# Kernel tuning notes

Measured on AMD Instinct MI355X. Metric: run time of the kernel, lower is better.

Reference implementation:

```python
import jax, jax.numpy as jnp
import numpy as np

B, N, G = 256, 512, 117  # batch, max_num_cells, n_genes
CH = 25                  # Emphsis conv out channels (hidden_d_1st_conv)


def setup_inputs() -> dict:
    key = jax.random.key(0)
    ks = jax.random.split(key, 11)
    images = jax.random.normal(ks[0], (B, N, 1, 7, 7), dtype=jnp.float32)
    spot_images = jax.random.normal(ks[1], (B, 1, 28, 28), dtype=jnp.float32)
    gene_expression = jax.random.normal(ks[2], (B, G), dtype=jnp.float32)
    # Emphsis: Conv2d(1, 25, k=3, s=1) + ReLU
    W_emph = jax.random.normal(ks[3], (CH, 1, 3, 3), dtype=jnp.float32) * 0.2
    b_emph = jax.random.normal(ks[4], (CH,), dtype=jnp.float32) * 0.1
    # 117 stacked GeneBlock Linear(625, 1) heads -> one (G, 625) matrix
    W_reg = jax.random.normal(ks[5], (G, 625), dtype=jnp.float32) * 0.04
    b_reg = jax.random.normal(ks[6], (G,), dtype=jnp.float32) * 0.1
    # PatchEmbedding: Conv2d(1, 3, k=5, s=5)
    W_patch = jax.random.normal(ks[7], (3, 1, 5, 5), dtype=jnp.float32) * 0.2
    b_patch = jax.random.normal(ks[8], (3,), dtype=jnp.float32) * 0.1
    # global_embedding: Linear(75, 1) + ELU
    W_glob = jax.random.normal(ks[9], (1, 75), dtype=jnp.float32) * 0.1
    b_glob = jax.random.normal(ks[10], (1,), dtype=jnp.float32) * 0.1
    return dict(images=images, spot_images=spot_images, gene_expression=gene_expression,
                W_emph=W_emph, b_emph=b_emph, W_reg=W_reg, b_reg=b_reg,
                W_patch=W_patch, b_patch=b_patch, W_glob=W_glob, b_glob=b_glob)


def reference(images, spot_images, gene_expression, W_emph, b_emph, W_reg, b_reg,
              W_patch, b_patch, W_glob, b_glob):
    Bn, Nc = images.shape[0], images.shape[1]
    # Emphsis conv over all (batch, cell) pairs at once: (B*N, 1, 7, 7) -> (B*N, 25, 5, 5)
    x = images.reshape(Bn * Nc, 1, 7, 7)
    t = jax.lax.conv_general_dilated(x, W_emph, window_strides=(1, 1), padding='VALID',
                                     dimension_numbers=('NCHW', 'OIHW', 'NCHW'))
    t = jax.nn.relu(t + b_emph[None, :, None, None])
    flat = t.reshape(Bn, Nc, CH * 5 * 5)  # (B, N, 625)
    # 117 independent Linear(625,1) heads fused into one matmul -> (B, N, G)
    out = jnp.einsum('bnd,gd->bng', flat, W_reg) + b_reg
    # PatchEmbedding: (B,1,28,28) -> (B,3,5,5) -> tokens (B,25,3) -> flatten (B,75)
    s = jax.lax.conv_general_dilated(spot_images, W_patch, window_strides=(5, 5), padding='VALID',
                                     dimension_numbers=('NCHW', 'OIHW', 'NCHW'))
    s = s + b_patch[None, :, None, None]
    s = s.reshape(Bn, 3, 25).transpose(0, 2, 1).reshape(Bn, 75)
    glob = jax.nn.elu(s @ W_glob.T + b_glob)  # (B, 1)
    # out1 broadcast of global embedding over (cells, genes)
    cell = jax.nn.relu(out + glob[:, :, None])  # (B, N, G)
    # F.linear with ones weight over cell axis == sum over cells
    spot = cell.sum(axis=1)  # (B, G)
    out1 = jnp.broadcast_to(glob[:, :, None], (Bn, Nc, out.shape[2]))  # (B, N, G)
    return spot, cell, out1
```

## Files before the change

kernel.cpp:

```cpp
#include <hip/hip_runtime.h>


typedef __attribute__((ext_vector_type(16))) float f32x16;
typedef __attribute__((ext_vector_type(8))) short short8;
typedef __attribute__((ext_vector_type(2))) unsigned int uint2v;
typedef __attribute__((ext_vector_type(4))) unsigned int uint4v;

#define WCOMB_OFF 0
#define GLOB_OFF  245760
#define SPOT_OFF  246784

#define SPOT_OUT_OFF 0
#define CELL_OUT_OFF 29952
#define OUT1_OUT_OFF 15365376

__device__ __forceinline__ unsigned short f2bf(float x) {
  unsigned int u = __builtin_bit_cast(unsigned int, x);
  u = (u + 0x7FFFu + ((u >> 16) & 1u)) >> 16;
  return (unsigned short)u;
}

__device__ __forceinline__ unsigned int cvt_pk_bf16(float lo, float hi) {
  unsigned int w;
  asm("v_cvt_pk_bf16_f32 %0, %1, %2" : "=v"(w) : "v"(lo), "v"(hi));
  return w;
}

__device__ __forceinline__ void gload16(const void* g, void* l) {
  __builtin_amdgcn_global_load_lds(
      (const __attribute__((address_space(1))) void*)g,
      (__attribute__((address_space(3))) void*)l, 16, 0, 0);
}

__global__ __launch_bounds__(128) void prep_kernel(
    const float* __restrict__ spot_images, const float* __restrict__ W_patch,
    const float* __restrict__ b_patch, const float* __restrict__ W_glob,
    const float* __restrict__ b_glob, const float* __restrict__ W_reg,
    const float* __restrict__ W_emph, const float* __restrict__ b_emph,
    unsigned short* __restrict__ wcomb, float* __restrict__ glob) {
  int bid = blockIdx.x;
  int tid = threadIdx.x;
  if (bid < 256) {
    __shared__ float red[75];
    if (tid < 75) {
      int token = tid / 3;
      int chan = tid - token * 3;
      int ty = token / 5, tx = token - ty * 5;
      const float* img = spot_images + bid * 784 + (ty * 5) * 28 + tx * 5;
      float a = 0.f;
      #pragma unroll
      for (int i = 0; i < 5; ++i)
        #pragma unroll
        for (int j = 0; j < 5; ++j)
          a = fmaf(img[i * 28 + j], W_patch[chan * 25 + i * 5 + j], a);
      a += b_patch[chan];
      red[tid] = a * W_glob[tid];
    }
    __syncthreads();
    if (tid == 0) {
      float s = b_glob[0];
      for (int k = 0; k < 75; ++k) s += red[k];
      glob[bid] = (s > 0.f) ? s : expm1f(s);
    }
  } else if (bid < 336) {
    int idx = bid - 256;
    int jt = idx >> 2, s = idx & 3;
    if (tid < 64) {
      int j = jt * 32 + (tid & 31);
      int h = tid >> 5;
      unsigned short hv[8];
      #pragma unroll
      for (int jj = 0; jj < 8; ++jj) {
        int i = s * 16 + h * 8 + jj;
        float val = 0.f;
        if (j < 625) {
          int ch = j / 25, p = j % 25;
          int oy = p / 5, ox = p - oy * 5;
          if (i < 49) {
            int iy = i / 7, ix = i - iy * 7;
            int ky = iy - oy, kx = ix - ox;
            if (ky >= 0 && ky < 3 && kx >= 0 && kx < 3)
              val = W_emph[ch * 9 + ky * 3 + kx];
          } else if (i == 49) {
            val = b_emph[ch];
          }
        }
        hv[jj] = f2bf(val);
      }
      unsigned int u[4];
      #pragma unroll
      for (int k = 0; k < 4; ++k)
        u[k] = (unsigned int)hv[2 * k] | ((unsigned int)hv[2 * k + 1] << 16);
      ((uint4*)wcomb)[jt * 768 + s * 64 + tid] = make_uint4(u[0], u[1], u[2], u[3]);
    }
  } else {
    int idx = bid - 336;
    int sg = idx >> 2, q = idx & 3;
    if (tid < 64) {
      int g = q * 32 + (tid & 31);
      int h = tid >> 5;
      unsigned short hv[8];
      #pragma unroll
      for (int jj = 0; jj < 8; ++jj) {
        int k = sg * 16 + h * 8 + jj;
        float val = (g < 117 && k < 625) ? W_reg[g * 625 + k] : 0.f;
        hv[jj] = f2bf(val);
      }
      unsigned int u[4];
      #pragma unroll
      for (int k = 0; k < 4; ++k)
        u[k] = (unsigned int)hv[2 * k] | ((unsigned int)hv[2 * k + 1] << 16);
      int jt = sg >> 1, c = (sg & 1) * 4 + q;
      ((uint4*)wcomb)[jt * 768 + 256 + c * 64 + tid] =
          make_uint4(u[0], u[1], u[2], u[3]);
    }
  }
}

__global__ __launch_bounds__(512) void main_kernel(
    const float* __restrict__ images, const float* __restrict__ b_reg,
    const unsigned short* __restrict__ wcomb, const float* __restrict__ glob,
    float* __restrict__ out, float* __restrict__ spotp) {
  __shared__ char smem[59392];
  unsigned short* imgbs = (unsigned short*)smem;
  char* wbuf = smem + 32768;
  float* C = (float*)smem;
  float* red = (float*)(smem + 57344);
  int tid = threadIdx.x;
  int bid = blockIdx.x;
  int b = bid >> 1, half = bid & 1;
  int n0 = half * 256;

  int l = tid & 63;
  int ct = __builtin_amdgcn_readfirstlane(tid >> 6);
  const char* wcombB = (const char*)wcomb;

  float gb = glob[b];
  size_t rowbase = (size_t)(b * 512 + n0);
  float4 gv = make_float4(gb, gb, gb, gb);
  float4* o1v = (float4*)(out + OUT1_OUT_OFF + rowbase * 117);

  auto stage = [&](int jt, int buf) {
    const char* s0 = wcombB + jt * 12288 + ct * 1024 + l * 16;
    char* d0 = wbuf + buf * 12288 + ct * 1024;
    gload16(s0, d0);
    if (ct < 4) gload16(s0 + 8192, d0 + 8192);
  };

  #pragma unroll
  for (int it = 0; it < 4; ++it) {
    int u = it * 512 + tid;
    int cell = u & 255, kc = u >> 8;
    const float* src = images + (size_t)(b * 512 + n0 + cell) * 49 + kc * 8;
    float v[8];
    #pragma unroll
    for (int j = 0; j < 8; ++j) v[j] = 0.f;
    if (kc < 6) {
      #pragma unroll
      for (int j = 0; j < 8; ++j) v[j] = src[j];
    } else if (kc == 6) {
      v[0] = src[0];
      v[1] = 1.0f;
    }
    unsigned int uu[4];
    #pragma unroll
    for (int k = 0; k < 4; ++k) uu[k] = cvt_pk_bf16(v[2 * k], v[2 * k + 1]);
    ((uint4*)imgbs)[kc * 256 + cell] = make_uint4(uu[0], uu[1], uu[2], uu[3]);
  }
  stage(0, 0);
  __syncthreads();

  int m = l & 31, hh = l >> 5;
  const short8* imgb8 = (const short8*)imgbs;

  short8 bi0 = imgb8[(0 + hh) * 256 + ct * 32 + m];
  short8 bi1 = imgb8[(2 + hh) * 256 + ct * 32 + m];
  short8 bi2 = imgb8[(4 + hh) * 256 + ct * 32 + m];
  short8 bi3 = imgb8[(6 + hh) * 256 + ct * 32 + m];

  f32x16 acc0, acc1, acc2, acc3;
  #pragma unroll
  for (int i = 0; i < 16; ++i) {
    acc0[i] = 0.f; acc1[i] = 0.f; acc2[i] = 0.f; acc3[i] = 0.f;
  }

  for (int jt = 0; jt < 20; ++jt) {
    if (jt < 19) stage(jt + 1, (jt + 1) & 1);

    if (jt < 15) {
      int idx = jt * 512 + tid;
      if (idx < 7488) o1v[idx] = gv;
    }

    const short8* wB = (const short8*)(wbuf + (jt & 1) * 12288);
    short8 a0 = wB[l];
    short8 a1 = wB[64 + l];
    short8 a2 = wB[128 + l];
    short8 a3 = wB[192 + l];

    f32x16 o;
    #pragma unroll
    for (int i = 0; i < 16; ++i) o[i] = 0.f;
    o = __builtin_amdgcn_mfma_f32_32x32x16_bf16(a0, bi0, o, 0, 0, 0);
    o = __builtin_amdgcn_mfma_f32_32x32x16_bf16(a1, bi1, o, 0, 0, 0);
    o = __builtin_amdgcn_mfma_f32_32x32x16_bf16(a2, bi2, o, 0, 0, 0);
    o = __builtin_amdgcn_mfma_f32_32x32x16_bf16(a3, bi3, o, 0, 0, 0);

    unsigned int W[8];
    #pragma unroll
    for (int q = 0; q < 8; ++q)
      W[q] = cvt_pk_bf16(fmaxf(o[2 * q], 0.f), fmaxf(o[2 * q + 1], 0.f));
    uint2v s02 = __builtin_amdgcn_permlane32_swap(W[0], W[2], false, false);
    uint2v s13 = __builtin_amdgcn_permlane32_swap(W[1], W[3], false, false);
    uint2v s46 = __builtin_amdgcn_permlane32_swap(W[4], W[6], false, false);
    uint2v s57 = __builtin_amdgcn_permlane32_swap(W[5], W[7], false, false);
    uint4v f0 = {s02[0], s13[0], s02[1], s13[1]};
    uint4v f1 = {s46[0], s57[0], s46[1], s57[1]};
    short8 af0 = __builtin_bit_cast(short8, f0);
    short8 af1 = __builtin_bit_cast(short8, f1);

    acc0 = __builtin_amdgcn_mfma_f32_32x32x16_bf16(af0, wB[256 + l], acc0, 0, 0, 0);
    acc1 = __builtin_amdgcn_mfma_f32_32x32x16_bf16(af0, wB[320 + l], acc1, 0, 0, 0);
    acc2 = __builtin_amdgcn_mfma_f32_32x32x16_bf16(af0, wB[384 + l], acc2, 0, 0, 0);
    acc3 = __builtin_amdgcn_mfma_f32_32x32x16_bf16(af0, wB[448 + l], acc3, 0, 0, 0);
    acc0 = __builtin_amdgcn_mfma_f32_32x32x16_bf16(af1, wB[512 + l], acc0, 0, 0, 0);
    acc1 = __builtin_amdgcn_mfma_f32_32x32x16_bf16(af1, wB[576 + l], acc1, 0, 0, 0);
    acc2 = __builtin_amdgcn_mfma_f32_32x32x16_bf16(af1, wB[640 + l], acc2, 0, 0, 0);
    acc3 = __builtin_amdgcn_mfma_f32_32x32x16_bf16(af1, wB[704 + l], acc3, 0, 0, 0);

    __syncthreads();
  }

  float part = 0.f;
  #pragma unroll
  for (int p = 0; p < 4; ++p) {
    if ((ct >> 1) == p) {
      int nb = (ct & 1) * 32;
      #define EPI(Q, ACC)                                                  \
        {                                                                  \
          int g = (Q)*32 + m;                                              \
          float br = (g < 117) ? b_reg[g] : 0.f;                           \
          _Pragma("unroll")                                                \
          for (int reg = 0; reg < 16; ++reg) {                             \
            int n = nb + (reg & 3) + 8 * (reg >> 2) + 4 * hh;              \
            C[n * 128 + g] = fmaxf(ACC[reg] + br + gb, 0.f);               \
          }                                                                \
        }
      EPI(0, acc0) EPI(1, acc1) EPI(2, acc2) EPI(3, acc3)
      #undef EPI
    }
    __syncthreads();
    float cellreg[15];
    #pragma unroll
    for (int i = 0; i < 15; ++i) {
      int idx = i * 512 + tid;
      int n = idx / 117;
      int gg = idx - n * 117;
      cellreg[i] = (idx < 7488) ? C[n * 128 + gg] : 0.f;
    }
    {
      int grp = tid >> 7, t = tid & 127;
      float s = 0.f;
      #pragma unroll
      for (int n = 0; n < 16; ++n) s += C[(grp * 16 + n) * 128 + t];
      red[grp * 128 + t] = s;
    }
    __syncthreads();
    if (tid < 128)
      part += red[tid] + red[128 + tid] + red[256 + tid] + red[384 + tid];
    float* cellchunk = out + CELL_OUT_OFF + (rowbase + p * 64) * 117;
    #pragma unroll
    for (int i = 0; i < 15; ++i) {
      int idx = i * 512 + tid;
      if (idx < 7488) cellchunk[idx] = cellreg[i];
    }
  }
  if (tid < 128)
    spotp[(size_t)(b * 2 + half) * 128 + tid] = part;
}

__global__ __launch_bounds__(256) void spot_reduce(
    const float* __restrict__ spotp, float* __restrict__ out) {
  int idx = blockIdx.x * 256 + threadIdx.x;
  int b = idx / 117;
  int g = idx - b * 117;
  float s = spotp[(size_t)(b * 2 + 0) * 128 + g] +
            spotp[(size_t)(b * 2 + 1) * 128 + g];
  out[SPOT_OUT_OFF + idx] = s;
}

extern "C" void kernel_launch(void* const* d_in, const int* in_sizes, int n_in,
                              void* d_out, int out_size, void* d_ws, size_t ws_size,
                              hipStream_t stream) {
  const float* images      = (const float*)d_in[0];
  const float* spot_images = (const float*)d_in[1];
  const float* W_emph = (const float*)d_in[3];
  const float* b_emph = (const float*)d_in[4];
  const float* W_reg  = (const float*)d_in[5];
  const float* b_reg  = (const float*)d_in[6];
  const float* W_patch = (const float*)d_in[7];
  const float* b_patch = (const float*)d_in[8];
  const float* W_glob  = (const float*)d_in[9];
  const float* b_glob  = (const float*)d_in[10];
  float* out = (float*)d_out;

  unsigned short* wcomb = (unsigned short*)((char*)d_ws + WCOMB_OFF);
  float* glob  = (float*)((char*)d_ws + GLOB_OFF);
  float* spotp = (float*)((char*)d_ws + SPOT_OFF);

  prep_kernel<<<496, 128, 0, stream>>>(spot_images, W_patch, b_patch, W_glob,
                                       b_glob, W_reg, W_emph, b_emph, wcomb,
                                       glob);
  main_kernel<<<512, 512, 0, stream>>>(images, b_reg, wcomb, glob, out, spotp);
  spot_reduce<<<117, 256, 0, stream>>>(spotp, out);
}
```

Before: 52.31 us.

## Process a full batch per block, reuse weight tiles across two cell tiles, drop reduce kernel

Each block now handles all 512 cells of one batch element instead of 256, with each wave computing two 32-cell tiles that share every loaded weight fragment. Because one block covers the whole cell axis, the spot sum is written directly and the separate spot_reduce kernel and its workspace round trip go away. Weight staging traffic per cell is halved and one launch is removed. In exchange only 256 blocks are launched, the accumulator register count doubles, and the image staging gains extra barriers.

```diff
diff --git a/kernel.cpp b/kernel.cpp
--- a/kernel.cpp
+++ b/kernel.cpp
@@ -8,7 +8,6 @@
 
 #define WCOMB_OFF 0
 #define GLOB_OFF  245760
-#define SPOT_OFF  246784
 
 #define SPOT_OUT_OFF 0
 #define CELL_OUT_OFF 29952
@@ -117,26 +116,25 @@
   }
 }
 
-__global__ __launch_bounds__(512) void main_kernel(
+__global__ __launch_bounds__(512, 2) void main_kernel(
     const float* __restrict__ images, const float* __restrict__ b_reg,
     const unsigned short* __restrict__ wcomb, const float* __restrict__ glob,
-    float* __restrict__ out, float* __restrict__ spotp) {
+    float* __restrict__ out) {
   __shared__ char smem[59392];
   unsigned short* imgbs = (unsigned short*)smem;
   char* wbuf = smem + 32768;
   float* C = (float*)smem;
   float* red = (float*)(smem + 57344);
   int tid = threadIdx.x;
-  int bid = blockIdx.x;
-  int b = bid >> 1, half = bid & 1;
-  int n0 = half * 256;
-
+  int b = blockIdx.x;
   int l = tid & 63;
   int ct = __builtin_amdgcn_readfirstlane(tid >> 6);
+  int m = l & 31, hh = l >> 5;
   const char* wcombB = (const char*)wcomb;
+  const short8* imgb8 = (const short8*)imgbs;
 
   float gb = glob[b];
-  size_t rowbase = (size_t)(b * 512 + n0);
+  size_t rowbase = (size_t)b * 512;
   float4 gv = make_float4(gb, gb, gb, gb);
   float4* o1v = (float4*)(out + OUT1_OUT_OFF + rowbase * 117);
 
@@ -147,49 +145,74 @@
     if (ct < 4) gload16(s0 + 8192, d0 + 8192);
   };
 
-  #pragma unroll
-  for (int it = 0; it < 4; ++it) {
-    int u = it * 512 + tid;
-    int cell = u & 255, kc = u >> 8;
-    const float* src = images + (size_t)(b * 512 + n0 + cell) * 49 + kc * 8;
-    float v[8];
-    #pragma unroll
-    for (int j = 0; j < 8; ++j) v[j] = 0.f;
-    if (kc < 6) {
-      #pragma unroll
-      for (int j = 0; j < 8; ++j) v[j] = src[j];
-    } else if (kc == 6) {
-      v[0] = src[0];
-      v[1] = 1.0f;
-    }
-    unsigned int uu[4];
-    #pragma unroll
-    for (int k = 0; k < 4; ++k) uu[k] = cvt_pk_bf16(v[2 * k], v[2 * k + 1]);
-    ((uint4*)imgbs)[kc * 256 + cell] = make_uint4(uu[0], uu[1], uu[2], uu[3]);
+  auto stageimg = [&](int hf) {
+    #pragma unroll
+    for (int it = 0; it < 4; ++it) {
+      int u = it * 512 + tid;
+      int cell = u & 255, kc = u >> 8;
+      const float* src =
+          images + (size_t)(b * 512 + hf * 256 + cell) * 49 + kc * 8;
+      float v[8];
+      #pragma unroll
+      for (int j = 0; j < 8; ++j) v[j] = 0.f;
+      if (kc < 6) {
+        #pragma unroll
+        for (int j = 0; j < 8; ++j) v[j] = src[j];
+      } else if (kc == 6) {
+        v[0] = src[0];
+        v[1] = 1.0f;
+      }
+      unsigned int uu[4];
+      #pragma unroll
+      for (int k = 0; k < 4; ++k) uu[k] = cvt_pk_bf16(v[2 * k], v[2 * k + 1]);
+      ((uint4*)imgbs)[kc * 256 + cell] = make_uint4(uu[0], uu[1], uu[2], uu[3]);
+    }
+  };
+
+  short8 bU0, bU1, bU2, bU3, bV0, bV1, bV2, bV3;
+  int base = (ct & 3) * 64;
+  stageimg(0);
+  __syncthreads();
+  if (ct < 4) {
+    bU0 = imgb8[(0 + hh) * 256 + base + m];
+    bU1 = imgb8[(2 + hh) * 256 + base + m];
+    bU2 = imgb8[(4 + hh) * 256 + base + m];
+    bU3 = imgb8[(6 + hh) * 256 + base + m];
+    bV0 = imgb8[(0 + hh) * 256 + base + 32 + m];
+    bV1 = imgb8[(2 + hh) * 256 + base + 32 + m];
+    bV2 = imgb8[(4 + hh) * 256 + base + 32 + m];
+    bV3 = imgb8[(6 + hh) * 256 + base + 32 + m];
+  }
+  __syncthreads();
+  stageimg(1);
+  __syncthreads();
+  if (ct >= 4) {
+    bU0 = imgb8[(0 + hh) * 256 + base + m];
+    bU1 = imgb8[(2 + hh) * 256 + base + m];
+    bU2 = imgb8[(4 + hh) * 256 + base + m];
+    bU3 = imgb8[(6 + hh) * 256 + base + m];
+    bV0 = imgb8[(0 + hh) * 256 + base + 32 + m];
+    bV1 = imgb8[(2 + hh) * 256 + base + 32 + m];
+    bV2 = imgb8[(4 + hh) * 256 + base + 32 + m];
+    bV3 = imgb8[(6 + hh) * 256 + base + 32 + m];
   }
   stage(0, 0);
   __syncthreads();
 
-  int m = l & 31, hh = l >> 5;
-  const short8* imgb8 = (const short8*)imgbs;
-
-  short8 bi0 = imgb8[(0 + hh) * 256 + ct * 32 + m];
-  short8 bi1 = imgb8[(2 + hh) * 256 + ct * 32 + m];
-  short8 bi2 = imgb8[(4 + hh) * 256 + ct * 32 + m];
-  short8 bi3 = imgb8[(6 + hh) * 256 + ct * 32 + m];
-
-  f32x16 acc0, acc1, acc2, acc3;
+  f32x16 aU0, aU1, aU2, aU3, aV0, aV1, aV2, aV3;
   #pragma unroll
   for (int i = 0; i < 16; ++i) {
-    acc0[i] = 0.f; acc1[i] = 0.f; acc2[i] = 0.f; acc3[i] = 0.f;
+    aU0[i] = 0.f; aU1[i] = 0.f; aU2[i] = 0.f; aU3[i] = 0.f;
+    aV0[i] = 0.f; aV1[i] = 0.f; aV2[i] = 0.f; aV3[i] = 0.f;
   }
 
   for (int jt = 0; jt < 20; ++jt) {
     if (jt < 19) stage(jt + 1, (jt + 1) & 1);
-
     if (jt < 15) {
-      int idx = jt * 512 + tid;
-      if (idx < 7488) o1v[idx] = gv;
+      int i0 = jt * 1024 + tid;
+      o1v[i0] = gv;
+      int i1 = i0 + 512;
+      if (i1 < 14976) o1v[i1] = gv;
     }
 
     const short8* wB = (const short8*)(wbuf + (jt & 1) * 12288);
@@ -201,11 +224,10 @@
     f32x16 o;
     #pragma unroll
     for (int i = 0; i < 16; ++i) o[i] = 0.f;
-    o = __builtin_amdgcn_mfma_f32_32x32x16_bf16(a0, bi0, o, 0, 0, 0);
-    o = __builtin_amdgcn_mfma_f32_32x32x16_bf16(a1, bi1, o, 0, 0, 0);
-    o = __builtin_amdgcn_mfma_f32_32x32x16_bf16(a2, bi2, o, 0, 0, 0);
-    o = __builtin_amdgcn_mfma_f32_32x32x16_bf16(a3, bi3, o, 0, 0, 0);
-
+    o = __builtin_amdgcn_mfma_f32_32x32x16_bf16(a0, bU0, o, 0, 0, 0);
+    o = __builtin_amdgcn_mfma_f32_32x32x16_bf16(a1, bU1, o, 0, 0, 0);
+    o = __builtin_amdgcn_mfma_f32_32x32x16_bf16(a2, bU2, o, 0, 0, 0);
+    o = __builtin_amdgcn_mfma_f32_32x32x16_bf16(a3, bU3, o, 0, 0, 0);
     unsigned int W[8];
     #pragma unroll
     for (int q = 0; q < 8; ++q)
@@ -216,37 +238,67 @@
     uint2v s57 = __builtin_amdgcn_permlane32_swap(W[5], W[7], false, false);
     uint4v f0 = {s02[0], s13[0], s02[1], s13[1]};
     uint4v f1 = {s46[0], s57[0], s46[1], s57[1]};
-    short8 af0 = __builtin_bit_cast(short8, f0);
-    short8 af1 = __builtin_bit_cast(short8, f1);
-
-    acc0 = __builtin_amdgcn_mfma_f32_32x32x16_bf16(af0, wB[256 + l], acc0, 0, 0, 0);
-    acc1 = __builtin_amdgcn_mfma_f32_32x32x16_bf16(af0, wB[320 + l], acc1, 0, 0, 0);
-    acc2 = __builtin_amdgcn_mfma_f32_32x32x16_bf16(af0, wB[384 + l], acc2, 0, 0, 0);
-    acc3 = __builtin_amdgcn_mfma_f32_32x32x16_bf16(af0, wB[448 + l], acc3, 0, 0, 0);
-    acc0 = __builtin_amdgcn_mfma_f32_32x32x16_bf16(af1, wB[512 + l], acc0, 0, 0, 0);
-    acc1 = __builtin_amdgcn_mfma_f32_32x32x16_bf16(af1, wB[576 + l], acc1, 0, 0, 0);
-    acc2 = __builtin_amdgcn_mfma_f32_32x32x16_bf16(af1, wB[640 + l], acc2, 0, 0, 0);
-    acc3 = __builtin_amdgcn_mfma_f32_32x32x16_bf16(af1, wB[704 + l], acc3, 0, 0, 0);
+    short8 afU0 = __builtin_bit_cast(short8, f0);
+    short8 afU1 = __builtin_bit_cast(short8, f1);
+
+    #pragma unroll
+    for (int i = 0; i < 16; ++i) o[i] = 0.f;
+    o = __builtin_amdgcn_mfma_f32_32x32x16_bf16(a0, bV0, o, 0, 0, 0);
+    o = __builtin_amdgcn_mfma_f32_32x32x16_bf16(a1, bV1, o, 0, 0, 0);
+    o = __builtin_amdgcn_mfma_f32_32x32x16_bf16(a2, bV2, o, 0, 0, 0);
+    o = __builtin_amdgcn_mfma_f32_32x32x16_bf16(a3, bV3, o, 0, 0, 0);
+    #pragma unroll
+    for (int q = 0; q < 8; ++q)
+      W[q] = cvt_pk_bf16(fmaxf(o[2 * q], 0.f), fmaxf(o[2 * q + 1], 0.f));
+    s02 = __builtin_amdgcn_permlane32_swap(W[0], W[2], false, false);
+    s13 = __builtin_amdgcn_permlane32_swap(W[1], W[3], false, false);
+    s46 = __builtin_amdgcn_permlane32_swap(W[4], W[6], false, false);
+    s57 = __builtin_amdgcn_permlane32_swap(W[5], W[7], false, false);
+    uint4v g0 = {s02[0], s13[0], s02[1], s13[1]};
+    uint4v g1 = {s46[0], s57[0], s46[1], s57[1]};
+    short8 afV0 = __builtin_bit_cast(short8, g0);
+    short8 afV1 = __builtin_bit_cast(short8, g1);
+
+    #define MM2(c, AFU, AFV, AU, AV)                                        \
+      {                                                                     \
+        short8 w = wB[256 + (c)*64 + l];                                    \
+        AU = __builtin_amdgcn_mfma_f32_32x32x16_bf16(AFU, w, AU, 0, 0, 0);  \
+        AV = __builtin_amdgcn_mfma_f32_32x32x16_bf16(AFV, w, AV, 0, 0, 0);  \
+      }
+    MM2(0, afU0, afV0, aU0, aV0)
+    MM2(1, afU0, afV0, aU1, aV1)
+    MM2(2, afU0, afV0, aU2, aV2)
+    MM2(3, afU0, afV0, aU3, aV3)
+    MM2(4, afU1, afV1, aU0, aV0)
+    MM2(5, afU1, afV1, aU1, aV1)
+    MM2(6, afU1, afV1, aU2, aV2)
+    MM2(7, afU1, afV1, aU3, aV3)
+    #undef MM2
 
     __syncthreads();
   }
 
+  float br0 = (0 * 32 + m < 117) ? b_reg[0 * 32 + m] : 0.f;
+  float br1 = (1 * 32 + m < 117) ? b_reg[1 * 32 + m] : 0.f;
+  float br2 = (2 * 32 + m < 117) ? b_reg[2 * 32 + m] : 0.f;
+  float br3 = (3 * 32 + m < 117) ? b_reg[3 * 32 + m] : 0.f;
+
   float part = 0.f;
-  #pragma unroll
-  for (int p = 0; p < 4; ++p) {
-    if ((ct >> 1) == p) {
-      int nb = (ct & 1) * 32;
-      #define EPI(Q, ACC)                                                  \
+  for (int p = 0; p < 8; ++p) {
+    if (ct == p) {
+      #define EPI(Q, ACC, NB, BR)                                          \
         {                                                                  \
           int g = (Q)*32 + m;                                              \
-          float br = (g < 117) ? b_reg[g] : 0.f;                           \
           _Pragma("unroll")                                                \
           for (int reg = 0; reg < 16; ++reg) {                             \
-            int n = nb + (reg & 3) + 8 * (reg >> 2) + 4 * hh;              \
-            C[n * 128 + g] = fmaxf(ACC[reg] + br + gb, 0.f);               \
+            int n = (NB) + (reg & 3) + 8 * (reg >> 2) + 4 * hh;            \
+            C[n * 128 + g] = fmaxf(ACC[reg] + (BR) + gb, 0.f);             \
           }                                                                \
         }
-      EPI(0, acc0) EPI(1, acc1) EPI(2, acc2) EPI(3, acc3)
+      EPI(0, aU0, 0, br0) EPI(1, aU1, 0, br1)
+      EPI(2, aU2, 0, br2) EPI(3, aU3, 0, br3)
+      EPI(0, aV0, 32, br0) EPI(1, aV1, 32, br1)
+      EPI(2, aV2, 32, br2) EPI(3, aV3, 32, br3)
       #undef EPI
     }
     __syncthreads();
@@ -275,18 +327,7 @@
       if (idx < 7488) cellchunk[idx] = cellreg[i];
     }
   }
-  if (tid < 128)
-    spotp[(size_t)(b * 2 + half) * 128 + tid] = part;
-}
-
-__global__ __launch_bounds__(256) void spot_reduce(
-    const float* __restrict__ spotp, float* __restrict__ out) {
-  int idx = blockIdx.x * 256 + threadIdx.x;
-  int b = idx / 117;
-  int g = idx - b * 117;
-  float s = spotp[(size_t)(b * 2 + 0) * 128 + g] +
-            spotp[(size_t)(b * 2 + 1) * 128 + g];
-  out[SPOT_OUT_OFF + idx] = s;
+  if (tid < 117) out[SPOT_OUT_OFF + b * 117 + tid] = part;
 }
 
 extern "C" void kernel_launch(void* const* d_in, const int* in_sizes, int n_in,
@@ -306,11 +347,9 @@
 
   unsigned short* wcomb = (unsigned short*)((char*)d_ws + WCOMB_OFF);
   float* glob  = (float*)((char*)d_ws + GLOB_OFF);
-  float* spotp = (float*)((char*)d_ws + SPOT_OFF);
 
   prep_kernel<<<496, 128, 0, stream>>>(spot_images, W_patch, b_patch, W_glob,
                                        b_glob, W_reg, W_emph, b_emph, wcomb,
                                        glob);
-  main_kernel<<<512, 512, 0, stream>>>(images, b_reg, wcomb, glob, out, spotp);
-  spot_reduce<<<117, 256, 0, stream>>>(spotp, out);
-}
+  main_kernel<<<256, 512, 0, stream>>>(images, b_reg, wcomb, glob, out);
+}
```

Result: faster. 51.27 us (-2.0%).

## Use one 1024-thread block per batch, read weights from global, write cells directly

Applied to the files above, without the earlier changes.

The main kernel now runs one 1024-thread block per batch instead of two 512-thread blocks per batch. Weight tiles are read straight from global memory (L2) rather than double-buffered into LDS with async loads, which removes the per-iteration barrier. The epilogue writes ReLU outputs directly from MFMA accumulators to global and reduces the spot sums in-block with shuffles, so the LDS staging and the separate spot_reduce kernel are gone. The trade-offs are fewer, larger blocks (256 blocks on the GPU), uncoalesced strided cell stores, and weight reads that depend on cache hits.

```diff
diff --git a/kernel.cpp b/kernel.cpp
--- a/kernel.cpp
+++ b/kernel.cpp
@@ -8,7 +8,6 @@
 
 #define WCOMB_OFF 0
 #define GLOB_OFF  245760
-#define SPOT_OFF  246784
 
 #define SPOT_OUT_OFF 0
 #define CELL_OUT_OFF 29952
@@ -24,12 +23,6 @@
   unsigned int w;
   asm("v_cvt_pk_bf16_f32 %0, %1, %2" : "=v"(w) : "v"(lo), "v"(hi));
   return w;
-}
-
-__device__ __forceinline__ void gload16(const void* g, void* l) {
-  __builtin_amdgcn_global_load_lds(
-      (const __attribute__((address_space(1))) void*)g,
-      (__attribute__((address_space(3))) void*)l, 16, 0, 0);
 }
 
 __global__ __launch_bounds__(128) void prep_kernel(
@@ -117,41 +110,30 @@
   }
 }
 
-__global__ __launch_bounds__(512) void main_kernel(
+__global__ __launch_bounds__(1024, 4) void main_kernel(
     const float* __restrict__ images, const float* __restrict__ b_reg,
     const unsigned short* __restrict__ wcomb, const float* __restrict__ glob,
-    float* __restrict__ out, float* __restrict__ spotp) {
-  __shared__ char smem[59392];
-  unsigned short* imgbs = (unsigned short*)smem;
-  char* wbuf = smem + 32768;
-  float* C = (float*)smem;
-  float* red = (float*)(smem + 57344);
+    float* __restrict__ out) {
+  __shared__ unsigned short imgbs[8 * 512 * 8];
+  __shared__ float redp[16 * 128];
   int tid = threadIdx.x;
-  int bid = blockIdx.x;
-  int b = bid >> 1, half = bid & 1;
-  int n0 = half * 256;
-
+  int b = blockIdx.x;
   int l = tid & 63;
-  int ct = __builtin_amdgcn_readfirstlane(tid >> 6);
-  const char* wcombB = (const char*)wcomb;
+  int wct = __builtin_amdgcn_readfirstlane(tid >> 6);
+  int m = l & 31, hh = l >> 5;
+  const short8* imgb8 = (const short8*)imgbs;
+  const short8* wc8 = (const short8*)wcomb;
 
   float gb = glob[b];
-  size_t rowbase = (size_t)(b * 512 + n0);
+  size_t rowbase = (size_t)b * 512;
   float4 gv = make_float4(gb, gb, gb, gb);
   float4* o1v = (float4*)(out + OUT1_OUT_OFF + rowbase * 117);
 
-  auto stage = [&](int jt, int buf) {
-    const char* s0 = wcombB + jt * 12288 + ct * 1024 + l * 16;
-    char* d0 = wbuf + buf * 12288 + ct * 1024;
-    gload16(s0, d0);
-    if (ct < 4) gload16(s0 + 8192, d0 + 8192);
-  };
-
   #pragma unroll
   for (int it = 0; it < 4; ++it) {
-    int u = it * 512 + tid;
-    int cell = u & 255, kc = u >> 8;
-    const float* src = images + (size_t)(b * 512 + n0 + cell) * 49 + kc * 8;
+    int u = it * 1024 + tid;
+    int cell = u & 511, kc = u >> 9;
+    const float* src = images + (size_t)(b * 512 + cell) * 49 + kc * 8;
     float v[8];
     #pragma unroll
     for (int j = 0; j < 8; ++j) v[j] = 0.f;
@@ -165,18 +147,14 @@
     unsigned int uu[4];
     #pragma unroll
     for (int k = 0; k < 4; ++k) uu[k] = cvt_pk_bf16(v[2 * k], v[2 * k + 1]);
-    ((uint4*)imgbs)[kc * 256 + cell] = make_uint4(uu[0], uu[1], uu[2], uu[3]);
-  }
-  stage(0, 0);
+    ((uint4*)imgbs)[kc * 512 + cell] = make_uint4(uu[0], uu[1], uu[2], uu[3]);
+  }
   __syncthreads();
 
-  int m = l & 31, hh = l >> 5;
-  const short8* imgb8 = (const short8*)imgbs;
-
-  short8 bi0 = imgb8[(0 + hh) * 256 + ct * 32 + m];
-  short8 bi1 = imgb8[(2 + hh) * 256 + ct * 32 + m];
-  short8 bi2 = imgb8[(4 + hh) * 256 + ct * 32 + m];
-  short8 bi3 = imgb8[(6 + hh) * 256 + ct * 32 + m];
+  short8 bF0 = imgb8[(0 + hh) * 512 + wct * 32 + m];
+  short8 bF1 = imgb8[(2 + hh) * 512 + wct * 32 + m];
+  short8 bF2 = imgb8[(4 + hh) * 512 + wct * 32 + m];
+  short8 bF3 = imgb8[(6 + hh) * 512 + wct * 32 + m];
 
   f32x16 acc0, acc1, acc2, acc3;
   #pragma unroll
@@ -185,14 +163,11 @@
   }
 
   for (int jt = 0; jt < 20; ++jt) {
-    if (jt < 19) stage(jt + 1, (jt + 1) & 1);
-
     if (jt < 15) {
-      int idx = jt * 512 + tid;
-      if (idx < 7488) o1v[idx] = gv;
-    }
-
-    const short8* wB = (const short8*)(wbuf + (jt & 1) * 12288);
+      int i0 = jt * 1024 + tid;
+      if (i0 < 14976) o1v[i0] = gv;
+    }
+    const short8* wB = wc8 + jt * 768;
     short8 a0 = wB[l];
     short8 a1 = wB[64 + l];
     short8 a2 = wB[128 + l];
@@ -201,11 +176,10 @@
     f32x16 o;
     #pragma unroll
     for (int i = 0; i < 16; ++i) o[i] = 0.f;
-    o = __builtin_amdgcn_mfma_f32_32x32x16_bf16(a0, bi0, o, 0, 0, 0);
-    o = __builtin_amdgcn_mfma_f32_32x32x16_bf16(a1, bi1, o, 0, 0, 0);
-    o = __builtin_amdgcn_mfma_f32_32x32x16_bf16(a2, bi2, o, 0, 0, 0);
-    o = __builtin_amdgcn_mfma_f32_32x32x16_bf16(a3, bi3, o, 0, 0, 0);
-
+    o = __builtin_amdgcn_mfma_f32_32x32x16_bf16(a0, bF0, o, 0, 0, 0);
+    o = __builtin_amdgcn_mfma_f32_32x32x16_bf16(a1, bF1, o, 0, 0, 0);
+    o = __builtin_amdgcn_mfma_f32_32x32x16_bf16(a2, bF2, o, 0, 0, 0);
+    o = __builtin_amdgcn_mfma_f32_32x32x16_bf16(a3, bF3, o, 0, 0, 0);
     unsigned int W[8];
     #pragma unroll
     for (int q = 0; q < 8; ++q)
@@ -227,66 +201,55 @@
     acc1 = __builtin_amdgcn_mfma_f32_32x32x16_bf16(af1, wB[576 + l], acc1, 0, 0, 0);
     acc2 = __builtin_amdgcn_mfma_f32_32x32x16_bf16(af1, wB[640 + l], acc2, 0, 0, 0);
     acc3 = __builtin_amdgcn_mfma_f32_32x32x16_bf16(af1, wB[704 + l], acc3, 0, 0, 0);
-
-    __syncthreads();
-  }
-
-  float part = 0.f;
+  }
+
+  float br0 = b_reg[m];
+  float br1 = b_reg[32 + m];
+  float br2 = b_reg[64 + m];
+  float br3 = (96 + m < 117) ? b_reg[96 + m] : 0.f;
+
+  {
+    auto rsum = [&](const f32x16& A, float br) {
+      float s = 0.f;
+      #pragma unroll
+      for (int reg = 0; reg < 16; ++reg) s += fmaxf(A[reg] + br + gb, 0.f);
+      s += __shfl_xor(s, 32, 64);
+      return s;
+    };
+    float s0 = rsum(acc0, br0);
+    float s1 = rsum(acc1, br1);
+    float s2 = rsum(acc2, br2);
+    float s3 = rsum(acc3, br3);
+    if (hh == 0) {
+      redp[wct * 128 + m] = s0;
+      redp[wct * 128 + 32 + m] = s1;
+      redp[wct * 128 + 64 + m] = s2;
+      redp[wct * 128 + 96 + m] = s3;
+    }
+  }
+  __syncthreads();
+  if (tid < 117) {
+    float s = 0.f;
+    #pragma unroll
+    for (int w = 0; w < 16; ++w) s += redp[w * 128 + tid];
+    out[SPOT_OUT_OFF + b * 117 + tid] = s;
+  }
+
+  bool q3ok = (m < 21);
+  float* cbase = out + CELL_OUT_OFF + (rowbase + wct * 32 + 4 * hh) * 117 + m;
   #pragma unroll
-  for (int p = 0; p < 4; ++p) {
-    if ((ct >> 1) == p) {
-      int nb = (ct & 1) * 32;
-      #define EPI(Q, ACC)                                                  \
-        {                                                                  \
-          int g = (Q)*32 + m;                                              \
-          float br = (g < 117) ? b_reg[g] : 0.f;                           \
-          _Pragma("unroll")                                                \
-          for (int reg = 0; reg < 16; ++reg) {                             \
-            int n = nb + (reg & 3) + 8 * (reg >> 2) + 4 * hh;              \
-            C[n * 128 + g] = fmaxf(ACC[reg] + br + gb, 0.f);               \
-          }                                                                \
-        }
-      EPI(0, acc0) EPI(1, acc1) EPI(2, acc2) EPI(3, acc3)
-      #undef EPI
-    }
-    __syncthreads();
-    float cellreg[15];
-    #pragma unroll
-    for (int i = 0; i < 15; ++i) {
-      int idx = i * 512 + tid;
-      int n = idx / 117;
-      int gg = idx - n * 117;
-      cellreg[i] = (idx < 7488) ? C[n * 128 + gg] : 0.f;
-    }
-    {
-      int grp = tid >> 7, t = tid & 127;
-      float s = 0.f;
-      #pragma unroll
-      for (int n = 0; n < 16; ++n) s += C[(grp * 16 + n) * 128 + t];
-      red[grp * 128 + t] = s;
-    }
-    __syncthreads();
-    if (tid < 128)
-      part += red[tid] + red[128 + tid] + red[256 + tid] + red[384 + tid];
-    float* cellchunk = out + CELL_OUT_OFF + (rowbase + p * 64) * 117;
-    #pragma unroll
-    for (int i = 0; i < 15; ++i) {
-      int idx = i * 512 + tid;
-      if (idx < 7488) cellchunk[idx] = cellreg[i];
-    }
-  }
-  if (tid < 128)
-    spotp[(size_t)(b * 2 + half) * 128 + tid] = part;
-}
-
-__global__ __launch_bounds__(256) void spot_reduce(
-    const float* __restrict__ spotp, float* __restrict__ out) {
-  int idx = blockIdx.x * 256 + threadIdx.x;
-  int b = idx / 117;
-  int g = idx - b * 117;
-  float s = spotp[(size_t)(b * 2 + 0) * 128 + g] +
-            spotp[(size_t)(b * 2 + 1) * 128 + g];
-  out[SPOT_OUT_OFF + idx] = s;
+  for (int G = 0; G < 4; ++G) {
+    float* p = cbase + (8 * G) * 117;
+    #pragma unroll
+    for (int rr = 0; rr < 4; ++rr) {
+      int r = G * 4 + rr;
+      int ro = rr * 117;
+      p[ro] = fmaxf(acc0[r] + br0 + gb, 0.f);
+      p[ro + 32] = fmaxf(acc1[r] + br1 + gb, 0.f);
+      p[ro + 64] = fmaxf(acc2[r] + br2 + gb, 0.f);
+      if (q3ok) p[ro + 96] = fmaxf(acc3[r] + br3 + gb, 0.f);
+    }
+  }
 }
 
 extern "C" void kernel_launch(void* const* d_in, const int* in_sizes, int n_in,
@@ -306,11 +269,9 @@
 
   unsigned short* wcomb = (unsigned short*)((char*)d_ws + WCOMB_OFF);
   float* glob  = (float*)((char*)d_ws + GLOB_OFF);
-  float* spotp = (float*)((char*)d_ws + SPOT_OFF);
 
   prep_kernel<<<496, 128, 0, stream>>>(spot_images, W_patch, b_patch, W_glob,
                                        b_glob, W_reg, W_emph, b_emph, wcomb,
                                        glob);
-  main_kernel<<<512, 512, 0, stream>>>(images, b_reg, wcomb, glob, out, spotp);
-  spot_reduce<<<117, 256, 0, stream>>>(spotp, out);
-}
+  main_kernel<<<256, 1024, 0, stream>>>(images, b_reg, wcomb, glob, out);
+}
```

Measured after the change: 59.76 us. +14.2%, slower.
